# Performance work log

Measured on AMD Instinct MI355X. Metric: run time of the kernel, lower is better.

## Reference

```python
import jax, jax.numpy as jnp
import numpy as np

N = 100000
HEADS = 4
NHID = 32


def _gat_conv(x, src, dst, W, a_src, a_dst, b):
    # x: [N, Fin]; src/dst: [E'] (self-loops already appended)
    h = (x @ W).reshape(N, HEADS, NHID)                      # [N, H, D]
    al_src = jnp.einsum('nhd,hd->nh', h, a_src)              # [N, H]
    al_dst = jnp.einsum('nhd,hd->nh', h, a_dst)
    e = jax.nn.leaky_relu(al_src[src] + al_dst[dst], 0.2)    # [E', H]
    # segment softmax over incoming edges of each destination node
    m = jax.ops.segment_max(e, dst, num_segments=N)          # [N, H]
    ex = jnp.exp(e - m[dst])
    s = jax.ops.segment_sum(ex, dst, num_segments=N)         # [N, H]
    alpha = ex / (s[dst] + 1e-16)                            # [E', H]
    msg = h[src] * alpha[:, :, None]                         # [E', H, D]
    out = jax.ops.segment_sum(msg, dst, num_segments=N)      # [N, H, D]
    return out.reshape(N, HEADS * NHID) + b


def setup_inputs() -> dict:
    key = jax.random.key(0)
    ks = jax.random.split(key, 16)
    E = 1600000
    NFEAT, NCLASS = 128, 10
    width = HEADS * NHID  # 128
    sc = 0.1
    inp = {
        'x': jax.random.normal(ks[0], (N, NFEAT), jnp.float32),
        'edge_index': jax.random.randint(ks[1], (2, E), 0, N, jnp.int64)
            if jax.config.jax_enable_x64 else jax.random.randint(ks[1], (2, E), 0, N, jnp.int32),
        'W0': jax.random.normal(ks[2], (NFEAT, width), jnp.float32) * sc,
        'a_src0': jax.random.normal(ks[3], (HEADS, NHID), jnp.float32) * sc,
        'a_dst0': jax.random.normal(ks[4], (HEADS, NHID), jnp.float32) * sc,
        'b0': jnp.zeros((width,), jnp.float32),
        'W1': jax.random.normal(ks[5], (width, width), jnp.float32) * sc,
        'a_src1': jax.random.normal(ks[6], (HEADS, NHID), jnp.float32) * sc,
        'a_dst1': jax.random.normal(ks[7], (HEADS, NHID), jnp.float32) * sc,
        'b1': jnp.zeros((width,), jnp.float32),
        'W2': jax.random.normal(ks[8], (width, width), jnp.float32) * sc,
        'a_src2': jax.random.normal(ks[9], (HEADS, NHID), jnp.float32) * sc,
        'a_dst2': jax.random.normal(ks[10], (HEADS, NHID), jnp.float32) * sc,
        'b2': jnp.zeros((width,), jnp.float32),
        'fc_W': jax.random.normal(ks[11], (width, NCLASS), jnp.float32) * sc,
        'fc_b': jnp.zeros((NCLASS,), jnp.float32),
    }
    return inp


def reference(x, edge_index, W0, a_src0, a_dst0, b0, W1, a_src1, a_dst1, b1,
              W2, a_src2, a_dst2, b2, fc_W, fc_b):
    # PyG GATConv default add_self_loops=True
    loops = jnp.arange(N, dtype=edge_index.dtype)
    src = jnp.concatenate([edge_index[0], loops])
    dst = jnp.concatenate([edge_index[1], loops])
    h = x
    for (W, a_s, a_d, b) in ((W0, a_src0, a_dst0, b0),
                             (W1, a_src1, a_dst1, b1),
                             (W2, a_src2, a_dst2, b2)):
        h = jax.nn.elu(_gat_conv(h, src, dst, W, a_s, a_d, b))
        # F.dropout(training=False) -> identity
    logits = h @ fc_W + fc_b
    return jax.nn.log_softmax(logits, axis=1)
```

## Files before the change

kernel.cpp:

```cpp
#include <hip/hip_runtime.h>
#include <math.h>

#define NN 100000
#define FEAT 128
#define NHEAD 4
#define BSH 9
#define BNODES 512
#define NBUCK 196
#define BCAP 16384
#define PA_EPT 16
#define GTILES 6250
#define GEMMB 1563
#define HSTRIDE 136
#define SRCMASK 0x1FFFF

typedef unsigned int uint;
typedef unsigned short ushort;
typedef __attribute__((ext_vector_type(8))) short short8;
typedef __attribute__((ext_vector_type(4))) float fx4;

__device__ __forceinline__ float lrelu(float v) { return v > 0.f ? v : 0.2f * v; }

__device__ __forceinline__ ushort f2bf(float f) {
    uint u = __float_as_uint(f);
    return (ushort)((u + 0x7fffu + ((u >> 16) & 1u)) >> 16);
}
__device__ __forceinline__ float bf_lo(uint u) { return __uint_as_float(u << 16); }
__device__ __forceinline__ float bf_hi(uint u) { return __uint_as_float(u & 0xffff0000u); }

__device__ __forceinline__ short8 pack8f(const float* p) {
    float4 a = *(const float4*)p, b = *(const float4*)(p + 4);
    short8 v;
    v[0] = (short)f2bf(a.x); v[1] = (short)f2bf(a.y);
    v[2] = (short)f2bf(a.z); v[3] = (short)f2bf(a.w);
    v[4] = (short)f2bf(b.x); v[5] = (short)f2bf(b.y);
    v[6] = (short)f2bf(b.z); v[7] = (short)f2bf(b.w);
    return v;
}

#define AGGR_STEP(hv, wgt)                                                    \
    a0 = fmaf(wgt, bf_lo(hv.x), a0); a1 = fmaf(wgt, bf_hi(hv.x), a1);        \
    a2 = fmaf(wgt, bf_lo(hv.y), a2); a3 = fmaf(wgt, bf_hi(hv.y), a3);        \
    a4 = fmaf(wgt, bf_lo(hv.z), a4); a5 = fmaf(wgt, bf_hi(hv.z), a5);        \
    a6 = fmaf(wgt, bf_lo(hv.w), a6); a7 = fmaf(wgt, bf_hi(hv.w), a7);

#define PROC4(cv)                                                             \
    {                                                                         \
        int s0 = cv.x, s1 = cv.y, s2 = cv.z, s3 = cv.w;                       \
        float w0 = __expf(lrelu(al_s[s0*4 + head] + ald_h));                  \
        float w1 = __expf(lrelu(al_s[s1*4 + head] + ald_h));                  \
        float w2 = __expf(lrelu(al_s[s2*4 + head] + ald_h));                  \
        float w3 = __expf(lrelu(al_s[s3*4 + head] + ald_h));                  \
        uint4 h0 = ((const uint4*)(hbf + (size_t)s0 * FEAT))[lane];           \
        uint4 h1 = ((const uint4*)(hbf + (size_t)s1 * FEAT))[lane];           \
        uint4 h2 = ((const uint4*)(hbf + (size_t)s2 * FEAT))[lane];           \
        uint4 h3 = ((const uint4*)(hbf + (size_t)s3 * FEAT))[lane];           \
        ssum += (w0 + w1) + (w2 + w3);                                        \
        AGGR_STEP(h0, w0) AGGR_STEP(h1, w1) AGGR_STEP(h2, w2) AGGR_STEP(h3, w3) \
    }

#define PROC8(cva, cvb)                                                       \
    {                                                                         \
        int s0 = cva.x, s1 = cva.y, s2 = cva.z, s3 = cva.w;                   \
        int s4 = cvb.x, s5 = cvb.y, s6 = cvb.z, s7 = cvb.w;                   \
        uint4 h0 = ((const uint4*)(hbf + (size_t)s0 * FEAT))[lane];           \
        uint4 h1 = ((const uint4*)(hbf + (size_t)s1 * FEAT))[lane];           \
        uint4 h2 = ((const uint4*)(hbf + (size_t)s2 * FEAT))[lane];           \
        uint4 h3 = ((const uint4*)(hbf + (size_t)s3 * FEAT))[lane];           \
        uint4 h4 = ((const uint4*)(hbf + (size_t)s4 * FEAT))[lane];           \
        uint4 h5 = ((const uint4*)(hbf + (size_t)s5 * FEAT))[lane];           \
        uint4 h6 = ((const uint4*)(hbf + (size_t)s6 * FEAT))[lane];           \
        uint4 h7 = ((const uint4*)(hbf + (size_t)s7 * FEAT))[lane];           \
        float w0 = __expf(lrelu(al_s[s0*4 + head] + ald_h));                  \
        float w1 = __expf(lrelu(al_s[s1*4 + head] + ald_h));                  \
        float w2 = __expf(lrelu(al_s[s2*4 + head] + ald_h));                  \
        float w3 = __expf(lrelu(al_s[s3*4 + head] + ald_h));                  \
        float w4 = __expf(lrelu(al_s[s4*4 + head] + ald_h));                  \
        float w5 = __expf(lrelu(al_s[s5*4 + head] + ald_h));                  \
        float w6 = __expf(lrelu(al_s[s6*4 + head] + ald_h));                  \
        float w7 = __expf(lrelu(al_s[s7*4 + head] + ald_h));                  \
        ssum += ((w0 + w1) + (w2 + w3)) + ((w4 + w5) + (w6 + w7));            \
        AGGR_STEP(h0, w0) AGGR_STEP(h1, w1) AGGR_STEP(h2, w2) AGGR_STEP(h3, w3) \
        AGGR_STEP(h4, w4) AGGR_STEP(h5, w5) AGGR_STEP(h6, w6) AGGR_STEP(h7, w7) \
    }

__device__ __forceinline__ void aggr_node(
    const int* __restrict__ row_ptr, const int* __restrict__ colidx,
    const ushort* __restrict__ hbf, const float* __restrict__ al_s,
    const float* __restrict__ al_d, const float* __restrict__ bias,
    int node, int lane, float* __restrict__ o)
{
    const int head = lane >> 2;
    float ald_h = al_d[node * 4 + head];
    int beg = row_ptr[node], end = row_ptr[node + 1];

    float ssum = 0.f;
    float a0=0.f,a1=0.f,a2=0.f,a3=0.f,a4=0.f,a5=0.f,a6=0.f,a7=0.f;

    int p = beg;
    int4 ca, cb;
    if (p + 8 <= end) {
        ca = *(const int4*)&colidx[p];
        cb = *(const int4*)&colidx[p + 4];
    }
    while (p + 16 <= end) {
        int4 na = *(const int4*)&colidx[p + 8];
        int4 nb = *(const int4*)&colidx[p + 12];
        PROC8(ca, cb)
        ca = na; cb = nb;
        p += 8;
    }
    if (p + 8 <= end) { PROC8(ca, cb) p += 8; }
    if (p + 4 <= end) {
        int4 c4 = *(const int4*)&colidx[p];
        PROC4(c4)
        p += 4;
    }
    for (; p < end; ++p) {
        int sn = colidx[p];
        float wq = __expf(lrelu(al_s[sn*4 + head] + ald_h));
        uint4 hv = ((const uint4*)(hbf + (size_t)sn * FEAT))[lane];
        ssum += wq;
        AGGR_STEP(hv, wq)
    }

    float inv = 1.f / (ssum + 1e-16f);
    const float* bp = bias + lane * 8;
    float oo[8] = {a0,a1,a2,a3,a4,a5,a6,a7};
    #pragma unroll
    for (int k = 0; k < 8; ++k) {
        float v = oo[k] * inv + bp[k];
        o[k] = v > 0.f ? v : __expf(v) - 1.f;
    }
}

template <bool FP32IN>
__device__ __forceinline__ void gemm_body(
    const void* __restrict__ in, const float* __restrict__ W,
    const float* __restrict__ a_src, const float* __restrict__ a_dst,
    ushort* __restrict__ hbf, float* __restrict__ al_s, float* __restrict__ al_d,
    int bid)
{
    __shared__ __align__(16) ushort WA[FEAT * FEAT];
    const int t = threadIdx.x;
    const int lane = t & 63;
    const int node_l = lane & 15, q = lane >> 4;
    const int tile = bid * 4 + (t >> 6);
    const bool valid = tile < GTILES;
    const int n0 = tile * 16;

    short8 b0, b1, b2, b3;
    const ushort* inbf = (const ushort*)in;
    const float*  inf  = (const float*)in;
    if (valid) {
        if (FP32IN) {
            const float* rf = inf + (size_t)(n0 + node_l) * FEAT + q * 8;
            b0 = pack8f(rf);
            b1 = pack8f(rf + 32);
            b2 = pack8f(rf + 64);
            b3 = pack8f(rf + 96);
        } else {
            const ushort* rowp = inbf + (size_t)(n0 + node_l) * FEAT + q * 8;
            b0 = *(const short8*)(rowp);
            b1 = *(const short8*)(rowp + 32);
            b2 = *(const short8*)(rowp + 64);
            b3 = *(const short8*)(rowp + 96);
        }
    }

    for (int idx = t; idx < FEAT * FEAT; idx += 256) {
        int k = idx >> 7, m = idx & 127;
        int mt = m >> 4, kt = k >> 5, qq = (k >> 3) & 3, j = k & 7;
        int ln = qq * 16 + (m & 15);
        WA[((mt * 4 + kt) * 64 + ln) * 8 + j] = f2bf(W[idx]);
    }
    __syncthreads();
    if (!valid) return;

    fx4 zero = {0.f, 0.f, 0.f, 0.f};
    fx4 acc[8];
    #pragma unroll
    for (int mt = 0; mt < 8; ++mt) acc[mt] = zero;
    #pragma unroll
    for (int kt = 0; kt < 4; ++kt) {
        short8 b = (kt == 0) ? b0 : (kt == 1) ? b1 : (kt == 2) ? b2 : b3;
        #pragma unroll
        for (int mt = 0; mt < 8; ++mt) {
            short8 a = *(const short8*)&WA[((mt * 4 + kt) * 64 + lane) * 8];
            acc[mt] = __builtin_amdgcn_mfma_f32_16x16x32_bf16(a, b, acc[mt], 0, 0, 0);
        }
    }

    float ps[4] = {0.f, 0.f, 0.f, 0.f};
    float pd[4] = {0.f, 0.f, 0.f, 0.f};
    #pragma unroll
    for (int mt = 0; mt < 8; ++mt) {
        float4 as4 = *(const float4*)(a_src + mt * 16 + q * 4);
        float4 ad4 = *(const float4*)(a_dst + mt * 16 + q * 4);
        ps[mt >> 1] += acc[mt][0] * as4.x + acc[mt][1] * as4.y + acc[mt][2] * as4.z + acc[mt][3] * as4.w;
        pd[mt >> 1] += acc[mt][0] * ad4.x + acc[mt][1] * ad4.y + acc[mt][2] * ad4.z + acc[mt][3] * ad4.w;
        ushort4 hv;
        hv.x = f2bf(acc[mt][0]); hv.y = f2bf(acc[mt][1]);
        hv.z = f2bf(acc[mt][2]); hv.w = f2bf(acc[mt][3]);
        *(ushort4*)(hbf + (size_t)(n0 + node_l) * FEAT + mt * 16 + q * 4) = hv;
    }
    #pragma unroll
    for (int h = 0; h < 4; ++h) {
        ps[h] += __shfl_xor(ps[h], 16); ps[h] += __shfl_xor(ps[h], 32);
        pd[h] += __shfl_xor(pd[h], 16); pd[h] += __shfl_xor(pd[h], 32);
    }
    float vs = (q == 0) ? ps[0] : (q == 1) ? ps[1] : (q == 2) ? ps[2] : ps[3];
    float vd = (q == 0) ? pd[0] : (q == 1) ? pd[1] : (q == 2) ? pd[2] : pd[3];
    al_s[(n0 + node_l) * 4 + q] = vs;
    al_d[(n0 + node_l) * 4 + q] = vd;
}

__device__ __forceinline__ void phaseA_body(
    const int* __restrict__ ei, int E, int* bcursor, uint* __restrict__ pairs, int bid)
{
    __shared__ int lh[NBUCK], lb[NBUCK];
    int t = threadIdx.x;
    if (t < NBUCK) lh[t] = 0;
    __syncthreads();
    int base = bid * (256 * PA_EPT) + t;
    int s[PA_EPT], d[PA_EPT];
    #pragma unroll
    for (int k = 0; k < PA_EPT; ++k) {
        int i = base + k * 256;
        if (i < E)            { s[k] = ei[i]; d[k] = ei[E + i]; }
        else if (i < E + NN)  { s[k] = i - E; d[k] = s[k]; }
        else                  { s[k] = 0; d[k] = -1; }
        if (d[k] >= 0) atomicAdd(&lh[d[k] >> BSH], 1);
    }
    __syncthreads();
    if (t < NBUCK) {
        int c = lh[t];
        lb[t] = c ? atomicAdd(&bcursor[t], c) : 0;
        lh[t] = 0;
    }
    __syncthreads();
    #pragma unroll
    for (int k = 0; k < PA_EPT; ++k) {
        if (d[k] >= 0) {
            int b = d[k] >> BSH;
            int off = atomicAdd(&lh[b], 1);
            pairs[lb[b] + off] = ((uint)(d[k] & (BNODES - 1)) << 17) | (uint)s[k];
        }
    }
}

__global__ __launch_bounds__(256, 2) void gemm0_phaseA_kernel(
    const float* __restrict__ x, const float* __restrict__ W,
    const float* __restrict__ a_src, const float* __restrict__ a_dst,
    ushort* __restrict__ hbf, float* __restrict__ al_s, float* __restrict__ al_d,
    const int* __restrict__ ei, int E, int* bcursor, uint* __restrict__ pairs)
{
    if (blockIdx.x < GEMMB)
        gemm_body<true>(x, W, a_src, a_dst, hbf, al_s, al_d, blockIdx.x);
    else
        phaseA_body(ei, E, bcursor, pairs, blockIdx.x - GEMMB);
}

__global__ __launch_bounds__(256, 2) void aggr_gemm_fused_kernel(
    const int* __restrict__ row_ptr, const int* __restrict__ colidx,
    const ushort* __restrict__ hbf_in, const float* __restrict__ al_s_in,
    const float* __restrict__ al_d_in, const float* __restrict__ bias,
    const float* __restrict__ W, const float* __restrict__ a_src,
    const float* __restrict__ a_dst,
    ushort* __restrict__ hbf_out, float* __restrict__ al_s_out,
    float* __restrict__ al_d_out)
{
    __shared__ __align__(16) ushort WA[FEAT * FEAT];
    __shared__ __align__(16) ushort HS[4][16 * HSTRIDE];
    const int t = threadIdx.x;
    for (int idx = t; idx < FEAT * FEAT; idx += 256) {
        int k = idx >> 7, m = idx & 127;
        int mt = m >> 4, kt = k >> 5, qq = (k >> 3) & 3, j = k & 7;
        int ln = qq * 16 + (m & 15);
        WA[((mt * 4 + kt) * 64 + ln) * 8 + j] = f2bf(W[idx]);
    }
    __syncthreads();

    const int wv = t >> 6, lane = t & 63;
    const int tile = blockIdx.x * 4 + wv;
    if (tile >= GTILES) return;
    const int n0 = tile * 16;
    const int ng = lane >> 4, l16 = lane & 15;

    #pragma unroll 1
    for (int it = 0; it < 4; ++it) {
        int node = n0 + it * 4 + ng;
        float o[8];
        aggr_node(row_ptr, colidx, hbf_in, al_s_in, al_d_in, bias, node, l16, o);
        uint4 u;
        u.x = (uint)f2bf(o[0]) | ((uint)f2bf(o[1]) << 16);
        u.y = (uint)f2bf(o[2]) | ((uint)f2bf(o[3]) << 16);
        u.z = (uint)f2bf(o[4]) | ((uint)f2bf(o[5]) << 16);
        u.w = (uint)f2bf(o[6]) | ((uint)f2bf(o[7]) << 16);
        *(uint4*)&HS[wv][(it * 4 + ng) * HSTRIDE + l16 * 8] = u;
    }

    const int node_l = l16, q = ng;
    short8 b0 = *(const short8*)&HS[wv][node_l * HSTRIDE +      q * 8];
    short8 b1 = *(const short8*)&HS[wv][node_l * HSTRIDE + 32 + q * 8];
    short8 b2 = *(const short8*)&HS[wv][node_l * HSTRIDE + 64 + q * 8];
    short8 b3 = *(const short8*)&HS[wv][node_l * HSTRIDE + 96 + q * 8];

    fx4 zero = {0.f, 0.f, 0.f, 0.f};
    fx4 acc[8];
    #pragma unroll
    for (int mt = 0; mt < 8; ++mt) acc[mt] = zero;
    #pragma unroll
    for (int kt = 0; kt < 4; ++kt) {
        short8 b = (kt == 0) ? b0 : (kt == 1) ? b1 : (kt == 2) ? b2 : b3;
        #pragma unroll
        for (int mt = 0; mt < 8; ++mt) {
            short8 a = *(const short8*)&WA[((mt * 4 + kt) * 64 + lane) * 8];
            acc[mt] = __builtin_amdgcn_mfma_f32_16x16x32_bf16(a, b, acc[mt], 0, 0, 0);
        }
    }

    float ps[4] = {0.f, 0.f, 0.f, 0.f};
    float pd[4] = {0.f, 0.f, 0.f, 0.f};
    #pragma unroll
    for (int mt = 0; mt < 8; ++mt) {
        float4 as4 = *(const float4*)(a_src + mt * 16 + q * 4);
        float4 ad4 = *(const float4*)(a_dst + mt * 16 + q * 4);
        ps[mt >> 1] += acc[mt][0] * as4.x + acc[mt][1] * as4.y + acc[mt][2] * as4.z + acc[mt][3] * as4.w;
        pd[mt >> 1] += acc[mt][0] * ad4.x + acc[mt][1] * ad4.y + acc[mt][2] * ad4.z + acc[mt][3] * ad4.w;
        ushort4 hv;
        hv.x = f2bf(acc[mt][0]); hv.y = f2bf(acc[mt][1]);
        hv.z = f2bf(acc[mt][2]); hv.w = f2bf(acc[mt][3]);
        *(ushort4*)(hbf_out + (size_t)(n0 + node_l) * FEAT + mt * 16 + q * 4) = hv;
    }
    #pragma unroll
    for (int h = 0; h < 4; ++h) {
        ps[h] += __shfl_xor(ps[h], 16); ps[h] += __shfl_xor(ps[h], 32);
        pd[h] += __shfl_xor(pd[h], 16); pd[h] += __shfl_xor(pd[h], 32);
    }
    float vs = (q == 0) ? ps[0] : (q == 1) ? ps[1] : (q == 2) ? ps[2] : ps[3];
    float vd = (q == 0) ? pd[0] : (q == 1) ? pd[1] : (q == 2) ? pd[2] : pd[3];
    al_s_out[(n0 + node_l) * 4 + q] = vs;
    al_d_out[(n0 + node_l) * 4 + q] = vd;
}


__global__ __launch_bounds__(256) void bucket_hist_kernel(
    const int* __restrict__ ei, int E, int* bsize)
{
    __shared__ int lh[NBUCK];
    int t = threadIdx.x;
    if (t < NBUCK) lh[t] = 0;
    __syncthreads();
    int stride = gridDim.x * 256;
    for (int i = blockIdx.x * 256 + t; i < E + NN; i += stride) {
        int d = (i < E) ? ei[E + i] : (i - E);
        atomicAdd(&lh[d >> BSH], 1);
    }
    __syncthreads();
    if (t < NBUCK && lh[t]) atomicAdd(&bsize[t], lh[t]);
}

__global__ __launch_bounds__(256) void bucket_scan_kernel(
    const int* __restrict__ bsize, int* bbase, int* bcursor)
{
    __shared__ int sm[256];
    int t = threadIdx.x;
    int v = (t < NBUCK) ? bsize[t] : 0;
    sm[t] = v;
    __syncthreads();
    #pragma unroll
    for (int off = 1; off < 256; off <<= 1) {
        int x = (t >= off) ? sm[t - off] : 0;
        __syncthreads();
        sm[t] += x;
        __syncthreads();
    }
    if (t < NBUCK) {
        int excl = sm[t] - v;
        bbase[t] = excl;
        bcursor[t] = excl;
    }
    if (t == 255) bbase[NBUCK] = sm[255];
}

__global__ __launch_bounds__(256) void phaseB_kernel(
    const uint* __restrict__ pairs, const int* __restrict__ bbase,
    int* __restrict__ row_ptr, int* __restrict__ colidx, int EP)
{
    __shared__ int nh[BNODES];
    __shared__ int ex[BNODES];
    __shared__ int ss[256];
    __shared__ int img[BCAP];
    int b = blockIdx.x, t = threadIdx.x;
    int node0 = b << BSH;
    int nend = min(NN - node0, BNODES);
    int pb = bbase[b], pe = bbase[b + 1];
    int span = pe - pb;
    for (int j = t; j < BNODES; j += 256) nh[j] = 0;
    __syncthreads();
    for (int i = t; i < span; i += 256)
        atomicAdd(&nh[pairs[pb + i] >> 17], 1);
    __syncthreads();
    int v0 = nh[2 * t], v1 = nh[2 * t + 1];
    int psc = v0 + v1;
    ss[t] = psc;
    __syncthreads();
    #pragma unroll
    for (int off = 1; off < 256; off <<= 1) {
        int x = (t >= off) ? ss[t - off] : 0;
        __syncthreads();
        ss[t] += x;
        __syncthreads();
    }
    int ep = ss[t] - psc;
    ex[2 * t] = ep;
    ex[2 * t + 1] = ep + v0;
    __syncthreads();
    for (int j = t; j < nend; j += 256) row_ptr[node0 + j] = pb + ex[j];
    if (b == NBUCK - 1 && t == 0) row_ptr[NN] = EP;
    for (int j = t; j < BNODES; j += 256) nh[j] = ex[j];
    __syncthreads();
    if (span <= BCAP) {
        for (int i = t; i < span; i += 256) {
            uint p = pairs[pb + i];
            int pos = atomicAdd(&nh[p >> 17], 1);
            img[pos] = (int)(p & SRCMASK);
        }
        __syncthreads();
        for (int i = t; i < span; i += 256) colidx[pb + i] = img[i];
    } else {
        for (int i = t; i < span; i += 256) {
            uint p = pairs[pb + i];
            int pos = atomicAdd(&nh[p >> 17], 1);
            colidx[pb + pos] = (int)(p & SRCMASK);
        }
    }
}

__global__ __launch_bounds__(256) void aggr_fc_kernel(
    const int* __restrict__ row_ptr, const int* __restrict__ colidx,
    const ushort* __restrict__ hbf, const float* __restrict__ al_s,
    const float* __restrict__ al_d, const float* __restrict__ bias,
    const float* __restrict__ fcW, const float* __restrict__ fcb,
    float* __restrict__ logout)
{
    __shared__ float WT[10][FEAT];
    __shared__ float bl[10];
    int t = threadIdx.x;
    for (int i = t; i < FEAT * 10; i += 256) {
        int k = i / 10, c = i % 10;
        WT[c][k] = fcW[i];
    }
    if (t < 10) bl[t] = fcb[t];
    __syncthreads();

    int node = blockIdx.x * 16 + (t >> 4);
    int lane = t & 15;
    float o[8];
    aggr_node(row_ptr, colidx, hbf, al_s, al_d, bias, node, lane, o);

    float lg[10];
    #pragma unroll
    for (int c = 0; c < 10; ++c) {
        const float* wr = &WT[c][lane * 8];
        float4 wa = *(const float4*)(wr);
        float4 wb = *(const float4*)(wr + 4);
        float acc = fmaf(o[0], wa.x, fmaf(o[1], wa.y, fmaf(o[2], wa.z, o[3] * wa.w)));
        acc = fmaf(o[4], wb.x, fmaf(o[5], wb.y, fmaf(o[6], wb.z, fmaf(o[7], wb.w, acc))));
        lg[c] = acc;
    }
    #pragma unroll
    for (int c = 0; c < 10; ++c) {
        lg[c] += __shfl_xor(lg[c], 1, 16);
        lg[c] += __shfl_xor(lg[c], 2, 16);
        lg[c] += __shfl_xor(lg[c], 4, 16);
        lg[c] += __shfl_xor(lg[c], 8, 16);
    }
    if (lane == 0) {
        float mx = -1e30f;
        #pragma unroll
        for (int c = 0; c < 10; ++c) { lg[c] += bl[c]; mx = fmaxf(mx, lg[c]); }
        float se = 0.f;
        #pragma unroll
        for (int c = 0; c < 10; ++c) se += __expf(lg[c] - mx);
        float lse = mx + __logf(se);
        float2* op = (float2*)(logout + (size_t)node * 10);
        #pragma unroll
        for (int c = 0; c < 5; ++c)
            op[c] = make_float2(lg[2*c] - lse, lg[2*c + 1] - lse);
    }
}

extern "C" void kernel_launch(void* const* d_in, const int* in_sizes, int n_in,
                              void* d_out, int out_size, void* d_ws, size_t ws_size,
                              hipStream_t stream)
{
    const float* x   = (const float*)d_in[0];
    const int*   ei  = (const int*)d_in[1];
    const float* W[3]   = {(const float*)d_in[2], (const float*)d_in[6],  (const float*)d_in[10]};
    const float* asr[3] = {(const float*)d_in[3], (const float*)d_in[7],  (const float*)d_in[11]};
    const float* ads[3] = {(const float*)d_in[4], (const float*)d_in[8],  (const float*)d_in[12]};
    const float* bs[3]  = {(const float*)d_in[5], (const float*)d_in[9],  (const float*)d_in[13]};
    const float* fcW = (const float*)d_in[14];
    const float* fcb = (const float*)d_in[15];
    const int E  = in_sizes[1] / 2;
    const int EP = E + NN;

    ushort* hbfA = (ushort*)d_ws;
    ushort* hbfB = hbfA + (size_t)NN * FEAT;
    float* alsA  = (float*)(hbfB + (size_t)NN * FEAT);
    float* aldA  = alsA + (size_t)NN * NHEAD;
    float* alsB  = aldA + (size_t)NN * NHEAD;
    float* aldB  = alsB + (size_t)NN * NHEAD;
    int* row_ptr = (int*)(aldB + (size_t)NN * NHEAD);
    int* bsize   = row_ptr + NN + 1;
    int* bbase   = bsize + NBUCK;
    int* bcursor = bbase + NBUCK + 1;
    uint* pairs  = (uint*)(bcursor + NBUCK);
    int* colidx  = (int*)(pairs + (size_t)EP);

    const int pab = (EP + 256 * PA_EPT - 1) / (256 * PA_EPT);

    hipMemsetAsync(bsize, 0, NBUCK * sizeof(int), stream);
    bucket_hist_kernel<<<1024, 256, 0, stream>>>(ei, E, bsize);
    bucket_scan_kernel<<<1, 256, 0, stream>>>(bsize, bbase, bcursor);

    gemm0_phaseA_kernel<<<GEMMB + pab, 256, 0, stream>>>(
        x, W[0], asr[0], ads[0], hbfA, alsA, aldA, ei, E, bcursor, pairs);
    phaseB_kernel<<<NBUCK, 256, 0, stream>>>(pairs, bbase, row_ptr, colidx, EP);

    aggr_gemm_fused_kernel<<<GEMMB, 256, 0, stream>>>(
        row_ptr, colidx, hbfA, alsA, aldA, bs[0], W[1], asr[1], ads[1],
        hbfB, alsB, aldB);
    aggr_gemm_fused_kernel<<<GEMMB, 256, 0, stream>>>(
        row_ptr, colidx, hbfB, alsB, aldB, bs[1], W[2], asr[2], ads[2],
        hbfA, alsA, aldA);

    aggr_fc_kernel<<<(NN + 15) / 16, 256, 0, stream>>>(
        row_ptr, colidx, hbfA, alsA, aldA, bs[2], fcW, fcb, (float*)d_out);
}
```

Measured before the change: 499.0 us.

## Precompute bf16 MFMA-layout weights once and read them from global memory

The three layer weight matrices are converted to bf16 in the MFMA fragment layout once, inside the histogram kernel, using extra blocks. The GEMM and aggregation kernels then read fragments straight from global memory (L2-resident) instead of having every block rebuild a 32KB LDS copy and hit a __syncthreads. Dropping that LDS use lets the fused aggregation kernel raise its launch bound to 4 blocks per CU. The cost is that weight fragments become global loads inside the MFMA loop, which may add latency.

Result: no change. 496.9 us (-0.4%).

```diff
diff --git a/kernel.cpp b/kernel.cpp
--- a/kernel.cpp
+++ b/kernel.cpp
@@ -12,6 +12,8 @@
 #define GTILES 6250
 #define GEMMB 1563
 #define HSTRIDE 136
+#define HISTB 1024
+#define WPREPB 192
 #define SRCMASK 0x1FFFF
 
 typedef unsigned int uint;
@@ -134,63 +136,11 @@
     }
 }
 
-template <bool FP32IN>
-__device__ __forceinline__ void gemm_body(
-    const void* __restrict__ in, const float* __restrict__ W,
-    const float* __restrict__ a_src, const float* __restrict__ a_dst,
-    ushort* __restrict__ hbf, float* __restrict__ al_s, float* __restrict__ al_d,
-    int bid)
-{
-    __shared__ __align__(16) ushort WA[FEAT * FEAT];
-    const int t = threadIdx.x;
-    const int lane = t & 63;
-    const int node_l = lane & 15, q = lane >> 4;
-    const int tile = bid * 4 + (t >> 6);
-    const bool valid = tile < GTILES;
-    const int n0 = tile * 16;
-
-    short8 b0, b1, b2, b3;
-    const ushort* inbf = (const ushort*)in;
-    const float*  inf  = (const float*)in;
-    if (valid) {
-        if (FP32IN) {
-            const float* rf = inf + (size_t)(n0 + node_l) * FEAT + q * 8;
-            b0 = pack8f(rf);
-            b1 = pack8f(rf + 32);
-            b2 = pack8f(rf + 64);
-            b3 = pack8f(rf + 96);
-        } else {
-            const ushort* rowp = inbf + (size_t)(n0 + node_l) * FEAT + q * 8;
-            b0 = *(const short8*)(rowp);
-            b1 = *(const short8*)(rowp + 32);
-            b2 = *(const short8*)(rowp + 64);
-            b3 = *(const short8*)(rowp + 96);
-        }
-    }
-
-    for (int idx = t; idx < FEAT * FEAT; idx += 256) {
-        int k = idx >> 7, m = idx & 127;
-        int mt = m >> 4, kt = k >> 5, qq = (k >> 3) & 3, j = k & 7;
-        int ln = qq * 16 + (m & 15);
-        WA[((mt * 4 + kt) * 64 + ln) * 8 + j] = f2bf(W[idx]);
-    }
-    __syncthreads();
-    if (!valid) return;
-
-    fx4 zero = {0.f, 0.f, 0.f, 0.f};
-    fx4 acc[8];
-    #pragma unroll
-    for (int mt = 0; mt < 8; ++mt) acc[mt] = zero;
-    #pragma unroll
-    for (int kt = 0; kt < 4; ++kt) {
-        short8 b = (kt == 0) ? b0 : (kt == 1) ? b1 : (kt == 2) ? b2 : b3;
-        #pragma unroll
-        for (int mt = 0; mt < 8; ++mt) {
-            short8 a = *(const short8*)&WA[((mt * 4 + kt) * 64 + lane) * 8];
-            acc[mt] = __builtin_amdgcn_mfma_f32_16x16x32_bf16(a, b, acc[mt], 0, 0, 0);
-        }
-    }
-
+__device__ __forceinline__ void gemm_epilogue(
+    fx4* acc, const float* __restrict__ a_src, const float* __restrict__ a_dst,
+    ushort* __restrict__ hbf_out, float* __restrict__ al_s_out,
+    float* __restrict__ al_d_out, int n0, int node_l, int q)
+{
     float ps[4] = {0.f, 0.f, 0.f, 0.f};
     float pd[4] = {0.f, 0.f, 0.f, 0.f};
     #pragma unroll
@@ -202,7 +152,7 @@
         ushort4 hv;
         hv.x = f2bf(acc[mt][0]); hv.y = f2bf(acc[mt][1]);
         hv.z = f2bf(acc[mt][2]); hv.w = f2bf(acc[mt][3]);
-        *(ushort4*)(hbf + (size_t)(n0 + node_l) * FEAT + mt * 16 + q * 4) = hv;
+        *(ushort4*)(hbf_out + (size_t)(n0 + node_l) * FEAT + mt * 16 + q * 4) = hv;
     }
     #pragma unroll
     for (int h = 0; h < 4; ++h) {
@@ -211,8 +161,43 @@
     }
     float vs = (q == 0) ? ps[0] : (q == 1) ? ps[1] : (q == 2) ? ps[2] : ps[3];
     float vd = (q == 0) ? pd[0] : (q == 1) ? pd[1] : (q == 2) ? pd[2] : pd[3];
-    al_s[(n0 + node_l) * 4 + q] = vs;
-    al_d[(n0 + node_l) * 4 + q] = vd;
+    al_s_out[(n0 + node_l) * 4 + q] = vs;
+    al_d_out[(n0 + node_l) * 4 + q] = vd;
+}
+
+__device__ __forceinline__ void gemm0_body(
+    const float* __restrict__ x, const ushort* __restrict__ wb,
+    const float* __restrict__ a_src, const float* __restrict__ a_dst,
+    ushort* __restrict__ hbf, float* __restrict__ al_s, float* __restrict__ al_d,
+    int bid)
+{
+    const int t = threadIdx.x;
+    const int lane = t & 63;
+    const int node_l = lane & 15, q = lane >> 4;
+    const int tile = bid * 4 + (t >> 6);
+    if (tile >= GTILES) return;
+    const int n0 = tile * 16;
+
+    const float* rf = x + (size_t)(n0 + node_l) * FEAT + q * 8;
+    short8 b0 = pack8f(rf);
+    short8 b1 = pack8f(rf + 32);
+    short8 b2 = pack8f(rf + 64);
+    short8 b3 = pack8f(rf + 96);
+
+    fx4 zero = {0.f, 0.f, 0.f, 0.f};
+    fx4 acc[8];
+    #pragma unroll
+    for (int mt = 0; mt < 8; ++mt) acc[mt] = zero;
+    #pragma unroll
+    for (int kt = 0; kt < 4; ++kt) {
+        short8 b = (kt == 0) ? b0 : (kt == 1) ? b1 : (kt == 2) ? b2 : b3;
+        #pragma unroll
+        for (int mt = 0; mt < 8; ++mt) {
+            short8 a = *(const short8*)&wb[((mt * 4 + kt) * 64 + lane) * 8];
+            acc[mt] = __builtin_amdgcn_mfma_f32_16x16x32_bf16(a, b, acc[mt], 0, 0, 0);
+        }
+    }
+    gemm_epilogue(acc, a_src, a_dst, hbf, al_s, al_d, n0, node_l, q);
 }
 
 __device__ __forceinline__ void phaseA_body(
@@ -250,37 +235,28 @@
 }
 
 __global__ __launch_bounds__(256, 2) void gemm0_phaseA_kernel(
-    const float* __restrict__ x, const float* __restrict__ W,
+    const float* __restrict__ x, const ushort* __restrict__ w0b,
     const float* __restrict__ a_src, const float* __restrict__ a_dst,
     ushort* __restrict__ hbf, float* __restrict__ al_s, float* __restrict__ al_d,
     const int* __restrict__ ei, int E, int* bcursor, uint* __restrict__ pairs)
 {
     if (blockIdx.x < GEMMB)
-        gemm_body<true>(x, W, a_src, a_dst, hbf, al_s, al_d, blockIdx.x);
+        gemm0_body(x, w0b, a_src, a_dst, hbf, al_s, al_d, blockIdx.x);
     else
         phaseA_body(ei, E, bcursor, pairs, blockIdx.x - GEMMB);
 }
 
-__global__ __launch_bounds__(256, 2) void aggr_gemm_fused_kernel(
+__global__ __launch_bounds__(256, 4) void aggr_gemm_fused_kernel(
     const int* __restrict__ row_ptr, const int* __restrict__ colidx,
     const ushort* __restrict__ hbf_in, const float* __restrict__ al_s_in,
     const float* __restrict__ al_d_in, const float* __restrict__ bias,
-    const float* __restrict__ W, const float* __restrict__ a_src,
+    const ushort* __restrict__ wb, const float* __restrict__ a_src,
     const float* __restrict__ a_dst,
     ushort* __restrict__ hbf_out, float* __restrict__ al_s_out,
     float* __restrict__ al_d_out)
 {
-    __shared__ __align__(16) ushort WA[FEAT * FEAT];
     __shared__ __align__(16) ushort HS[4][16 * HSTRIDE];
     const int t = threadIdx.x;
-    for (int idx = t; idx < FEAT * FEAT; idx += 256) {
-        int k = idx >> 7, m = idx & 127;
-        int mt = m >> 4, kt = k >> 5, qq = (k >> 3) & 3, j = k & 7;
-        int ln = qq * 16 + (m & 15);
-        WA[((mt * 4 + kt) * 64 + ln) * 8 + j] = f2bf(W[idx]);
-    }
-    __syncthreads();
-
     const int wv = t >> 6, lane = t & 63;
     const int tile = blockIdx.x * 4 + wv;
     if (tile >= GTILES) return;
@@ -299,6 +275,7 @@
         u.w = (uint)f2bf(o[6]) | ((uint)f2bf(o[7]) << 16);
         *(uint4*)&HS[wv][(it * 4 + ng) * HSTRIDE + l16 * 8] = u;
     }
+    __builtin_amdgcn_sched_barrier(0);
 
     const int node_l = l16, q = ng;
     short8 b0 = *(const short8*)&HS[wv][node_l * HSTRIDE +      q * 8];
@@ -315,50 +292,43 @@
         short8 b = (kt == 0) ? b0 : (kt == 1) ? b1 : (kt == 2) ? b2 : b3;
         #pragma unroll
         for (int mt = 0; mt < 8; ++mt) {
-            short8 a = *(const short8*)&WA[((mt * 4 + kt) * 64 + lane) * 8];
+            short8 a = *(const short8*)&wb[((mt * 4 + kt) * 64 + lane) * 8];
             acc[mt] = __builtin_amdgcn_mfma_f32_16x16x32_bf16(a, b, acc[mt], 0, 0, 0);
         }
     }
-
-    float ps[4] = {0.f, 0.f, 0.f, 0.f};
-    float pd[4] = {0.f, 0.f, 0.f, 0.f};
-    #pragma unroll
-    for (int mt = 0; mt < 8; ++mt) {
-        float4 as4 = *(const float4*)(a_src + mt * 16 + q * 4);
-        float4 ad4 = *(const float4*)(a_dst + mt * 16 + q * 4);
-        ps[mt >> 1] += acc[mt][0] * as4.x + acc[mt][1] * as4.y + acc[mt][2] * as4.z + acc[mt][3] * as4.w;
-        pd[mt >> 1] += acc[mt][0] * ad4.x + acc[mt][1] * ad4.y + acc[mt][2] * ad4.z + acc[mt][3] * ad4.w;
-        ushort4 hv;
-        hv.x = f2bf(acc[mt][0]); hv.y = f2bf(acc[mt][1]);
-        hv.z = f2bf(acc[mt][2]); hv.w = f2bf(acc[mt][3]);
-        *(ushort4*)(hbf_out + (size_t)(n0 + node_l) * FEAT + mt * 16 + q * 4) = hv;
-    }
-    #pragma unroll
-    for (int h = 0; h < 4; ++h) {
-        ps[h] += __shfl_xor(ps[h], 16); ps[h] += __shfl_xor(ps[h], 32);
-        pd[h] += __shfl_xor(pd[h], 16); pd[h] += __shfl_xor(pd[h], 32);
-    }
-    float vs = (q == 0) ? ps[0] : (q == 1) ? ps[1] : (q == 2) ? ps[2] : ps[3];
-    float vd = (q == 0) ? pd[0] : (q == 1) ? pd[1] : (q == 2) ? pd[2] : pd[3];
-    al_s_out[(n0 + node_l) * 4 + q] = vs;
-    al_d_out[(n0 + node_l) * 4 + q] = vd;
-}
-
-
-__global__ __launch_bounds__(256) void bucket_hist_kernel(
-    const int* __restrict__ ei, int E, int* bsize)
-{
-    __shared__ int lh[NBUCK];
+    gemm_epilogue(acc, a_src, a_dst, hbf_out, al_s_out, al_d_out, n0, node_l, q);
+}
+
+
+__global__ __launch_bounds__(256) void hist_wprep_kernel(
+    const int* __restrict__ ei, int E, int* bsize,
+    const float* __restrict__ W0, const float* __restrict__ W1,
+    const float* __restrict__ W2,
+    ushort* __restrict__ wb0, ushort* __restrict__ wb1, ushort* __restrict__ wb2)
+{
     int t = threadIdx.x;
-    if (t < NBUCK) lh[t] = 0;
-    __syncthreads();
-    int stride = gridDim.x * 256;
-    for (int i = blockIdx.x * 256 + t; i < E + NN; i += stride) {
-        int d = (i < E) ? ei[E + i] : (i - E);
-        atomicAdd(&lh[d >> BSH], 1);
-    }
-    __syncthreads();
-    if (t < NBUCK && lh[t]) atomicAdd(&bsize[t], lh[t]);
+    if (blockIdx.x < HISTB) {
+        __shared__ int lh[NBUCK];
+        if (t < NBUCK) lh[t] = 0;
+        __syncthreads();
+        int stride = HISTB * 256;
+        for (int i = blockIdx.x * 256 + t; i < E + NN; i += stride) {
+            int d = (i < E) ? ei[E + i] : (i - E);
+            atomicAdd(&lh[d >> BSH], 1);
+        }
+        __syncthreads();
+        if (t < NBUCK && lh[t]) atomicAdd(&bsize[t], lh[t]);
+    } else {
+        int b = blockIdx.x - HISTB;
+        int mat = b >> 6;
+        int idx = ((b & 63) << 8) | t;
+        const float* Wm = (mat == 0) ? W0 : (mat == 1) ? W1 : W2;
+        ushort* wbm     = (mat == 0) ? wb0 : (mat == 1) ? wb1 : wb2;
+        int k = idx >> 7, m = idx & 127;
+        int mt = m >> 4, kt = k >> 5, qq = (k >> 3) & 3, j = k & 7;
+        int ln = qq * 16 + (m & 15);
+        wbm[((mt * 4 + kt) * 64 + ln) * 8 + j] = f2bf(Wm[idx]);
+    }
 }
 
 __global__ __launch_bounds__(256) void bucket_scan_kernel(
@@ -517,24 +487,29 @@
     int* bsize   = row_ptr + NN + 1;
     int* bbase   = bsize + NBUCK;
     int* bcursor = bbase + NBUCK + 1;
-    uint* pairs  = (uint*)(bcursor + NBUCK);
+    uintptr_t pw = ((uintptr_t)(bcursor + NBUCK) + 15) & ~(uintptr_t)15;
+    ushort* wb0  = (ushort*)pw;
+    ushort* wb1  = wb0 + FEAT * FEAT;
+    ushort* wb2  = wb1 + FEAT * FEAT;
+    uint* pairs  = (uint*)(wb2 + FEAT * FEAT);
     int* colidx  = (int*)(pairs + (size_t)EP);
 
     const int pab = (EP + 256 * PA_EPT - 1) / (256 * PA_EPT);
 
     hipMemsetAsync(bsize, 0, NBUCK * sizeof(int), stream);
-    bucket_hist_kernel<<<1024, 256, 0, stream>>>(ei, E, bsize);
+    hist_wprep_kernel<<<HISTB + WPREPB, 256, 0, stream>>>(
+        ei, E, bsize, W[0], W[1], W[2], wb0, wb1, wb2);
     bucket_scan_kernel<<<1, 256, 0, stream>>>(bsize, bbase, bcursor);
 
     gemm0_phaseA_kernel<<<GEMMB + pab, 256, 0, stream>>>(
-        x, W[0], asr[0], ads[0], hbfA, alsA, aldA, ei, E, bcursor, pairs);
+        x, wb0, asr[0], ads[0], hbfA, alsA, aldA, ei, E, bcursor, pairs);
     phaseB_kernel<<<NBUCK, 256, 0, stream>>>(pairs, bbase, row_ptr, colidx, EP);
 
     aggr_gemm_fused_kernel<<<GEMMB, 256, 0, stream>>>(
-        row_ptr, colidx, hbfA, alsA, aldA, bs[0], W[1], asr[1], ads[1],
+        row_ptr, colidx, hbfA, alsA, aldA, bs[0], wb1, asr[1], ads[1],
         hbfB, alsB, aldB);
     aggr_gemm_fused_kernel<<<GEMMB, 256, 0, stream>>>(
-        row_ptr, colidx, hbfB, alsB, aldB, bs[1], W[2], asr[2], ads[2],
+        row_ptr, colidx, hbfB, alsB, aldB, bs[1], wb2, asr[2], ads[2],
         hbfA, alsA, aldA);
 
     aggr_fc_kernel<<<(NN + 15) / 16, 256, 0, stream>>>(
```
